# Kernel tuning notes

Measured on AMD Instinct MI355X. Metric: run time of the kernel, lower is better.

Reference implementation:

```python
import jax, jax.numpy as jnp
import numpy as np

E = 8       # num experts
TOPK = 2    # top-k routing
R = 16      # lora rank
D = 2048    # d_model
F = 5632    # ffn hidden
B, S = 4, 2048


def setup_inputs() -> dict:
    key = jax.random.key(0)
    ks = jax.random.split(key, 11)
    sc = 0.02
    return {
        "x": jax.random.normal(ks[0], (B, S, D), jnp.float32),
        "gate_w": jax.random.normal(ks[1], (E, D), jnp.float32) * sc,
        "W1": jax.random.normal(ks[2], (F, D), jnp.float32) * sc,
        "W3": jax.random.normal(ks[3], (F, D), jnp.float32) * sc,
        "W2": jax.random.normal(ks[4], (D, F), jnp.float32) * sc,
        "A1": jax.random.normal(ks[5], (E, R, D), jnp.float32) * sc,
        "B1": jax.random.normal(ks[6], (E, F, R), jnp.float32) * sc,
        "A3": jax.random.normal(ks[7], (E, R, D), jnp.float32) * sc,
        "B3": jax.random.normal(ks[8], (E, F, R), jnp.float32) * sc,
        "A2": jax.random.normal(ks[9], (E, R, F), jnp.float32) * sc,
        "B2": jax.random.normal(ks[10], (E, D, R), jnp.float32) * sc,
    }


def reference(x, gate_w, W1, W3, W2, A1, B1, A3, B3, A2, B2):
    b, s, d = x.shape
    h = x.reshape(-1, d)                              # [T, D] tokens
    # --- BasicMoe routing (fp32 softmax, top-k, renormalize) ---
    router_logits = h @ gate_w.T                      # [T, E]
    probs = jax.nn.softmax(router_logits.astype(jnp.float32), axis=-1)
    w, sel = jax.lax.top_k(probs, TOPK)               # [T, K]
    w = w / jnp.sum(w, axis=-1, keepdims=True)
    w = w.astype(h.dtype)
    # per-token per-expert combine coefficient [T, E] (0 if not routed)
    coef = jnp.sum(jax.nn.one_hot(sel, E, dtype=w.dtype) * w[..., None], axis=1)
    # --- shared base projections (expert-independent) ---
    base1 = h @ W1.T                                  # [T, F]
    base3 = h @ W3.T                                  # [T, F]
    out = jnp.zeros_like(h)
    # small fixed loop over experts; dense-masked equivalent of gather/scatter
    for e in range(E):
        u1 = base1 + (h @ A1[e].T) @ B1[e].T          # w1 + loraB1(loraA1(x))
        u3 = base3 + (h @ A3[e].T) @ B3[e].T
        g = jax.nn.silu(u1) * u3                      # SwiGLU gate
        y = g @ W2.T + (g @ A2[e].T) @ B2[e].T        # w2 + lora2
        out = out + coef[:, e:e + 1] * y
    return out.reshape(b, s, d), router_logits
```

## Files before the change

kernel.cpp:

```cpp
#include <hip/hip_runtime.h>
#include <hip/hip_bf16.h>
#include <stdint.h>

#define TT   8192
#define DD   2048
#define FF   5632
#define EE   8
#define RR   16
#define NALL 11520
#define KE   5760
#define NPAIR 16384

typedef float  f32x4  __attribute__((ext_vector_type(4)));
typedef __bf16 bf16x8 __attribute__((ext_vector_type(8)));
typedef __bf16 bf16x4 __attribute__((ext_vector_type(4)));

#define AS1CAST(p) ((__attribute__((address_space(1))) void*)(p))
#define AS3CAST(p) ((__attribute__((address_space(3))) void*)(p))

__global__ __launch_bounds__(256) void cvt_f32_bf16(const float* __restrict__ src,
                                                    __bf16* __restrict__ dst, int n4) {
    int stride = gridDim.x * 256;
    for (int i = blockIdx.x * 256 + threadIdx.x; i < n4; i += stride) {
        float4 v = ((const float4*)src)[i];
        bf16x4 o = {(__bf16)v.x, (__bf16)v.y, (__bf16)v.z, (__bf16)v.w};
        ((bf16x4*)dst)[i] = o;
    }
}

__global__ __launch_bounds__(256) void cvt_A13(const float* __restrict__ A1,
                                               const float* __restrict__ A3,
                                               __bf16* __restrict__ dst) {
    int i = blockIdx.x * 256 + threadIdx.x;
    int col4 = i & 511;
    int j = i >> 9;
    int e = j >> 5, l = j & 31;
    const float* src = (l < 16) ? (A1 + (size_t)(e * 16 + l) * DD)
                                : (A3 + (size_t)(e * 16 + (l - 16)) * DD);
    float4 v = ((const float4*)src)[col4];
    bf16x4 o = {(__bf16)v.x, (__bf16)v.y, (__bf16)v.z, (__bf16)v.w};
    ((bf16x4*)(dst + (size_t)j * DD))[col4] = o;
}

__global__ __launch_bounds__(256) void cvt_A2t(const float* __restrict__ A2,
                                               __bf16* __restrict__ A2t) {
    int i = blockIdx.x * 256 + threadIdx.x;
    int f = i % FF;
    int r = (i / FF) % RR;
    int e = i / (FF * RR);
    A2t[((size_t)e * FF + f) * RR + r] = (__bf16)A2[i];
}

__global__ __launch_bounds__(256) void cvt_W2ext(const float* __restrict__ W2,
                                                 const float* __restrict__ B2,
                                                 __bf16* __restrict__ dst) {
    const int n4 = DD * KE / 4;
    int stride = gridDim.x * 256;
    for (int i = blockIdx.x * 256 + threadIdx.x; i < n4; i += stride) {
        int j = (i % (KE / 4)) * 4;
        int d = i / (KE / 4);
        float4 v;
        if (j < FF) {
            v = *(const float4*)(W2 + (size_t)d * FF + j);
        } else {
            int o = j - FF;
            int e = o >> 4, r = o & 15;
            const float* b = B2 + ((size_t)e * DD + d) * RR + r;
            v.x = b[0]; v.y = b[1]; v.z = b[2]; v.w = b[3];
        }
        bf16x4 o4 = {(__bf16)v.x, (__bf16)v.y, (__bf16)v.z, (__bf16)v.w};
        ((bf16x4*)dst)[i] = o4;
    }
}

__global__ __launch_bounds__(256) void router_k(const float* __restrict__ x,
                                                const float* __restrict__ gw,
                                                float* __restrict__ logits,
                                                int* __restrict__ pair_e,
                                                float* __restrict__ pair_w) {
    int t = blockIdx.x * 4 + (threadIdx.x >> 6);
    int lane = threadIdx.x & 63;
    const float* xr = x + (size_t)t * DD;
    float acc[EE];
#pragma unroll
    for (int e = 0; e < EE; e++) acc[e] = 0.f;
    for (int d = lane; d < DD; d += 64) {
        float xv = xr[d];
#pragma unroll
        for (int e = 0; e < EE; e++) acc[e] += xv * gw[e * DD + d];
    }
#pragma unroll
    for (int off = 32; off > 0; off >>= 1) {
#pragma unroll
        for (int e = 0; e < EE; e++) acc[e] += __shfl_down(acc[e], off, 64);
    }
    if (lane == 0) {
        float mx = acc[0];
#pragma unroll
        for (int e = 1; e < EE; e++) mx = fmaxf(mx, acc[e]);
        float p[EE];
#pragma unroll
        for (int e = 0; e < EE; e++) p[e] = __expf(acc[e] - mx);
        int e0 = 0;
#pragma unroll
        for (int e = 1; e < EE; e++) if (p[e] > p[e0]) e0 = e;
        int e1 = (e0 == 0) ? 1 : 0;
#pragma unroll
        for (int e = 0; e < EE; e++) if (e != e0 && p[e] > p[e1]) e1 = e;
        float s = p[e0] + p[e1];
        pair_e[2 * t] = e0;     pair_e[2 * t + 1] = e1;
        pair_w[2 * t] = p[e0] / s; pair_w[2 * t + 1] = p[e1] / s;
#pragma unroll
        for (int e = 0; e < EE; e++) logits[(size_t)t * EE + e] = acc[e];
    }
}

template <int OUT_BF16>
__global__ __launch_bounds__(512, 2) void gemm256(const __bf16* __restrict__ A,
                                                  const __bf16* __restrict__ B,
                                                  void* __restrict__ Cv,
                                                  int M, int N, int K) {
    __shared__ __align__(16) __bf16 lds[8][8192];
    char* const sbase = (char*)&lds[0][0];
    const int tid = threadIdx.x;
    const int w = tid >> 6, lane = tid & 63;
    const int lrow = lane & 15, lq = lane >> 4;
    const int wr = w >> 2, wc = w & 3;

    const int gx = gridDim.x;
    const int nwg = gx * gridDim.y;
    const int orig = blockIdx.x + blockIdx.y * gx;
    const int q8 = nwg >> 3, r8 = nwg & 7;
    const int xcd = orig & 7, sid = orig >> 3;
    const int nid = (xcd < r8 ? xcd * (q8 + 1) : r8 * (q8 + 1) + (xcd - r8) * q8) + sid;
    const int m0 = (nid % gx) * 256;
    const int n0 = (nid / gx) * 256;

    const size_t ldb = (size_t)K * 2;
    const int rq0 = w * 16 + (lane >> 3);
    const int cbs = ((lane & 7) * 16) ^ (((rq0 >> 2) & 1) << 5);
    const char* gA0 = (const char*)A + (size_t)(m0 + rq0) * ldb + cbs;
    const char* gA1 = gA0 + (size_t)128 * ldb;
    const char* gB0 = (const char*)B + (size_t)(n0 + rq0) * ldb + cbs;
    const char* gB1 = gB0 + (size_t)128 * ldb;
    const int wseg = w * 2048;

    const int sb = ((lrow >> 2) & 1) << 5;
    const int aoff = lrow * 128 + ((lq * 16) ^ sb);
    const int boff = ((wc & 1) * 64 + lrow) * 128 + ((lq * 16) ^ sb);
    const int abuf = wr;
    const int bbuf = 2 + (wc >> 1);

    f32x4 acc[8][4] = {};
    bf16x8 aR[4][2], aS[4][2], bR[2][2], bS[2][2];

#define GLDS(gp, lo) __builtin_amdgcn_global_load_lds(AS1CAST((void*)(gp)), AS3CAST(sbase + (lo)), 16, 0, 0)
#define STAGEM(gp, bufmh) do { const char* _g = (gp); \
        GLDS(_g, (bufmh) * 16384 + wseg); \
        GLDS(_g + 8 * ldb, (bufmh) * 16384 + wseg + 1024); } while (0)
#define LDAf(c, i, ks) (*(const bf16x8*)(sbase + ((c) * 4 + abuf) * 16384 + aoff + (i) * 2048 + (ks) * 64))
#define LDBf(c, j, ks) (*(const bf16x8*)(sbase + ((c) * 4 + bbuf) * 16384 + boff + (j) * 2048 + (ks) * 64))
#define MM(i, j, fa, fb) acc[i][j] = __builtin_amdgcn_mfma_f32_16x16x32_bf16(fa, fb, acc[i][j], 0, 0, 0)
#define PH_MID() do { __builtin_amdgcn_s_barrier(); \
        asm volatile("s_waitcnt lgkmcnt(0)" ::: "memory"); \
        __builtin_amdgcn_sched_barrier(0); \
        __builtin_amdgcn_s_setprio(1); } while (0)
#define PH_END() do { __builtin_amdgcn_s_setprio(0); \
        __builtin_amdgcn_s_barrier(); } while (0)

#define DO4(c, kBC, kAC) do { \
    _Pragma("unroll") for (int i = 0; i < 4; i++) { aR[i][0] = LDAf(c, i, 0); aR[i][1] = LDAf(c, i, 1); } \
    _Pragma("unroll") for (int j = 0; j < 2; j++) { bR[j][0] = LDBf(c, j, 0); bR[j][1] = LDBf(c, j, 1); } \
    STAGEM(gB0 + (size_t)(kBC) * 128, ((c) ^ 1) * 4 + 2); \
    PH_MID(); \
    _Pragma("unroll") for (int i = 0; i < 4; i++) \
    _Pragma("unroll") for (int j = 0; j < 2; j++) { MM(i, j, aR[i][0], bR[j][0]); MM(i, j, aR[i][1], bR[j][1]); } \
    PH_END(); \
    _Pragma("unroll") for (int i = 0; i < 4; i++) { aS[i][0] = LDAf(c, 4 + i, 0); aS[i][1] = LDAf(c, 4 + i, 1); } \
    STAGEM(gB1 + (size_t)(kBC) * 128, ((c) ^ 1) * 4 + 3); \
    PH_MID(); \
    _Pragma("unroll") for (int i = 0; i < 4; i++) \
    _Pragma("unroll") for (int j = 0; j < 2; j++) { MM(4 + i, j, aS[i][0], bR[j][0]); MM(4 + i, j, aS[i][1], bR[j][1]); } \
    PH_END(); \
    _Pragma("unroll") for (int j = 0; j < 2; j++) { bS[j][0] = LDBf(c, 2 + j, 0); bS[j][1] = LDBf(c, 2 + j, 1); } \
    STAGEM(gA0 + (size_t)(kAC) * 128, (c) * 4 + 0); \
    PH_MID(); \
    _Pragma("unroll") for (int i = 0; i < 4; i++) \
    _Pragma("unroll") for (int j = 0; j < 2; j++) { MM(i, 2 + j, aR[i][0], bS[j][0]); MM(i, 2 + j, aR[i][1], bS[j][1]); } \
    PH_END(); \
    STAGEM(gA1 + (size_t)(kAC) * 128, (c) * 4 + 1); \
    asm volatile("s_waitcnt vmcnt(4)" ::: "memory"); \
    PH_MID(); \
    _Pragma("unroll") for (int i = 0; i < 4; i++) \
    _Pragma("unroll") for (int j = 0; j < 2; j++) { MM(4 + i, 2 + j, aS[i][0], bS[j][0]); MM(4 + i, 2 + j, aS[i][1], bS[j][1]); } \
    PH_END(); \
} while (0)

    const int NT = K >> 6;
    const int NI = NT >> 1;

    STAGEM(gA0, 0); STAGEM(gA1, 1); STAGEM(gB0, 2); STAGEM(gB1, 3);
    STAGEM(gA0 + 128, 4); STAGEM(gA1 + 128, 5);
    asm volatile("s_waitcnt vmcnt(4)" ::: "memory");
    __builtin_amdgcn_s_barrier();

    for (int it = 0; it < NI; it++) {
        int k2 = 2 * it + 2; if (k2 > NT - 1) k2 = NT - 1;
        int k3 = 2 * it + 3; if (k3 > NT - 1) k3 = NT - 1;
        DO4(0, 2 * it + 1, k2);
        DO4(1, k2, k3);
    }

    asm volatile("s_waitcnt vmcnt(0)" ::: "memory");

#undef DO4
#undef PH_END
#undef PH_MID
#undef MM
#undef LDBf
#undef LDAf
#undef STAGEM
#undef GLDS

#pragma unroll
    for (int i = 0; i < 8; i++)
#pragma unroll
        for (int j = 0; j < 4; j++)
#pragma unroll
            for (int r = 0; r < 4; r++) {
                int row = m0 + wr * 128 + i * 16 + lq * 4 + r;
                int col = n0 + wc * 64 + j * 16 + lrow;
                float v = acc[i][j][r];
                if (OUT_BF16) ((__bf16*)Cv)[(size_t)row * N + col] = (__bf16)v;
                else          ((float*)Cv)[(size_t)row * N + col] = v;
            }
}

__global__ __launch_bounds__(256) void g_build_tok(const __bf16* __restrict__ base,
                                                   const __bf16* __restrict__ B1t,
                                                   const __bf16* __restrict__ B3t,
                                                   const __bf16* __restrict__ A2t,
                                                   const int* __restrict__ pair_e,
                                                   const float* __restrict__ pair_w,
                                                   __bf16* __restrict__ G,
                                                   int t0) {
    const int wave = threadIdx.x >> 6, lane = threadIdx.x & 63;
    const int lt = blockIdx.x * 4 + wave;
    const int t = t0 + lt;
    const int e0 = pair_e[2 * t], e1 = pair_e[2 * t + 1];
    const float w0 = pair_w[2 * t], w1 = pair_w[2 * t + 1];
    const __bf16* brow = base + (size_t)lt * NALL;

    float ha1a[16], ha3a[16], ha1b[16], ha3b[16];
    {
        const bf16x8* pa = (const bf16x8*)(brow + 2 * FF + e0 * 32);
        const bf16x8* pb = (const bf16x8*)(brow + 2 * FF + e1 * 32);
        bf16x8 a0 = pa[0], a1 = pa[1], a2v = pa[2], a3v = pa[3];
        bf16x8 b0 = pb[0], b1v = pb[1], b2v = pb[2], b3v = pb[3];
#pragma unroll
        for (int r = 0; r < 8; r++) {
            ha1a[r] = (float)a0[r];  ha1a[8 + r] = (float)a1[r];
            ha3a[r] = (float)a2v[r]; ha3a[8 + r] = (float)a3v[r];
            ha1b[r] = (float)b0[r];  ha1b[8 + r] = (float)b1v[r];
            ha3b[r] = (float)b2v[r]; ha3b[8 + r] = (float)b3v[r];
        }
    }
    const __bf16* B1a = B1t + (size_t)e0 * FF * RR;
    const __bf16* B3a = B3t + (size_t)e0 * FF * RR;
    const __bf16* A2a = A2t + (size_t)e0 * FF * RR;
    const __bf16* B1b = B1t + (size_t)e1 * FF * RR;
    const __bf16* B3b = B3t + (size_t)e1 * FF * RR;
    const __bf16* A2b = A2t + (size_t)e1 * FF * RR;
    __bf16* Grow = G + (size_t)lt * KE;

    float ga0[16], ga1[16];
#pragma unroll
    for (int r = 0; r < 16; r++) { ga0[r] = 0.f; ga1[r] = 0.f; }

    for (int f = lane; f < FF; f += 64) {
        const size_t fo = (size_t)f * RR;
        const bf16x8* p;
        p = (const bf16x8*)(B1a + fo); bf16x8 b1l = p[0], b1h = p[1];
        p = (const bf16x8*)(B3a + fo); bf16x8 b3l = p[0], b3h = p[1];
        p = (const bf16x8*)(B1b + fo); bf16x8 c1l = p[0], c1h = p[1];
        p = (const bf16x8*)(B3b + fo); bf16x8 c3l = p[0], c3h = p[1];
        float bb1 = (float)brow[f], bb3 = (float)brow[FF + f];
        float u1a = bb1, u3a = bb3, u1b = bb1, u3b = bb3;
#pragma unroll
        for (int r = 0; r < 8; r++) {
            u1a += ha1a[r] * (float)b1l[r] + ha1a[8 + r] * (float)b1h[r];
            u3a += ha3a[r] * (float)b3l[r] + ha3a[8 + r] * (float)b3h[r];
            u1b += ha1b[r] * (float)c1l[r] + ha1b[8 + r] * (float)c1h[r];
            u3b += ha3b[r] * (float)c3l[r] + ha3b[8 + r] * (float)c3h[r];
        }
        float g0 = (u1a / (1.f + __expf(-u1a))) * u3a;
        float g1 = (u1b / (1.f + __expf(-u1b))) * u3b;
        Grow[f] = (__bf16)(w0 * g0 + w1 * g1);
        p = (const bf16x8*)(A2a + fo); bf16x8 a2l = p[0], a2h = p[1];
        p = (const bf16x8*)(A2b + fo); bf16x8 a4l = p[0], a4h = p[1];
#pragma unroll
        for (int r = 0; r < 8; r++) {
            ga0[r]     += g0 * (float)a2l[r];
            ga0[8 + r] += g0 * (float)a2h[r];
            ga1[r]     += g1 * (float)a4l[r];
            ga1[8 + r] += g1 * (float)a4h[r];
        }
    }
#pragma unroll
    for (int off = 32; off > 0; off >>= 1) {
#pragma unroll
        for (int r = 0; r < 16; r++) {
            ga0[r] += __shfl_down(ga0[r], off, 64);
            ga1[r] += __shfl_down(ga1[r], off, 64);
        }
    }
    if (lane == 0) {
        __bf16* tail = Grow + FF;
        bf16x8 z = {};
#pragma unroll
        for (int e = 0; e < EE; e++) {
            if (e == e0) {
                bf16x8 lo, hi;
#pragma unroll
                for (int r = 0; r < 8; r++) { lo[r] = (__bf16)(w0 * ga0[r]); hi[r] = (__bf16)(w0 * ga0[8 + r]); }
                ((bf16x8*)(tail + e * 16))[0] = lo; ((bf16x8*)(tail + e * 16))[1] = hi;
            } else if (e == e1) {
                bf16x8 lo, hi;
#pragma unroll
                for (int r = 0; r < 8; r++) { lo[r] = (__bf16)(w1 * ga1[r]); hi[r] = (__bf16)(w1 * ga1[8 + r]); }
                ((bf16x8*)(tail + e * 16))[0] = lo; ((bf16x8*)(tail + e * 16))[1] = hi;
            } else {
                ((bf16x8*)(tail + e * 16))[0] = z; ((bf16x8*)(tail + e * 16))[1] = z;
            }
        }
    }
}

extern "C" void kernel_launch(void* const* d_in, const int* in_sizes, int n_in,
                              void* d_out, int out_size, void* d_ws, size_t ws_size,
                              hipStream_t stream) {
    const float* x  = (const float*)d_in[0];
    const float* gw = (const float*)d_in[1];
    const float* W1 = (const float*)d_in[2];
    const float* W3 = (const float*)d_in[3];
    const float* W2 = (const float*)d_in[4];
    const float* A1 = (const float*)d_in[5];
    const float* B1 = (const float*)d_in[6];
    const float* A3 = (const float*)d_in[7];
    const float* B3 = (const float*)d_in[8];
    const float* A2 = (const float*)d_in[9];
    const float* B2 = (const float*)d_in[10];

    float* out    = (float*)d_out;
    float* logits = out + (size_t)TT * DD;

    char* ws = (char*)d_ws;
    size_t off = 0;
    auto carve = [&](size_t bytes) {
        char* p = ws + off;
        off += (bytes + 255) & ~(size_t)255;
        return p;
    };
    auto pad = [](size_t b) { return (b + 255) & ~(size_t)255; };

    __bf16* B1b   = (__bf16*)carve((size_t)EE * FF * RR * 2);
    __bf16* B3b   = (__bf16*)carve((size_t)EE * FF * RR * 2);
    __bf16* A2t   = (__bf16*)carve((size_t)EE * FF * RR * 2);
    int*    pair_e = (int*)carve((size_t)NPAIR * 4);
    float*  pair_w = (float*)carve((size_t)NPAIR * 4);
    char*   WREG  = carve((size_t)NALL * DD * 2);
    __bf16* W_all = (__bf16*)WREG;
    size_t base0 = off;

    int C = 0, full = 0;
    {
        const int cand[5] = {4096, 2048, 1024, 512, 256};
        for (int ci = 0; ci < 5; ci++) {
            int c = cand[ci];
            size_t need = base0 + pad((size_t)TT * KE * 2)
                        + pad((size_t)c * DD * 2) + pad((size_t)c * NALL * 2);
            if (need <= ws_size) { full = 1; C = c; break; }
        }
    }
    __bf16* Gbuf = nullptr; __bf16* base_c; __bf16* h_c; __bf16* W2e; __bf16* G_c = nullptr;
    if (full) {
        Gbuf   = (__bf16*)carve((size_t)TT * KE * 2);
        h_c    = (__bf16*)carve((size_t)C * DD * 2);
        base_c = (__bf16*)carve((size_t)C * NALL * 2);
        W2e    = (__bf16*)WREG;
    } else {
        W2e = (__bf16*)carve((size_t)DD * KE * 2);
        C = 2048;
        while (C > 256) {
            size_t need = off + pad((size_t)C * DD * 2)
                        + pad((size_t)C * NALL * 2) + pad((size_t)C * KE * 2);
            if (need <= ws_size) break;
            C >>= 1;
        }
        h_c    = (__bf16*)carve((size_t)C * DD * 2);
        base_c = (__bf16*)carve((size_t)C * NALL * 2);
        G_c    = (__bf16*)carve((size_t)C * KE * 2);
    }

    cvt_f32_bf16<<<1024, 256, 0, stream>>>(W1, W_all, FF * DD / 4);
    cvt_f32_bf16<<<1024, 256, 0, stream>>>(W3, W_all + (size_t)FF * DD, FF * DD / 4);
    cvt_A13<<<512, 256, 0, stream>>>(A1, A3, W_all + (size_t)2 * FF * DD);
    cvt_f32_bf16<<<512, 256, 0, stream>>>(B1, B1b, EE * FF * RR / 4);
    cvt_f32_bf16<<<512, 256, 0, stream>>>(B3, B3b, EE * FF * RR / 4);
    cvt_A2t<<<EE * RR * FF / 256, 256, 0, stream>>>(A2, A2t);
    if (!full) cvt_W2ext<<<2048, 256, 0, stream>>>(W2, B2, W2e);

    router_k<<<TT / 4, 256, 0, stream>>>(x, gw, logits, pair_e, pair_w);

    for (int t0 = 0; t0 < TT; t0 += C) {
        cvt_f32_bf16<<<1024, 256, 0, stream>>>(x + (size_t)t0 * DD, h_c, C * DD / 4);
        gemm256<1><<<dim3(C / 256, NALL / 256), 512, 0, stream>>>(
            h_c, W_all, base_c, C, NALL, DD);
        __bf16* Gp = full ? (Gbuf + (size_t)t0 * KE) : G_c;
        g_build_tok<<<C / 4, 256, 0, stream>>>(base_c, B1b, B3b, A2t, pair_e, pair_w, Gp, t0);
        if (!full) {
            gemm256<0><<<dim3(C / 256, DD / 256), 512, 0, stream>>>(
                G_c, W2e, out + (size_t)t0 * DD, C, DD, KE);
        }
    }

    if (full) {
        cvt_W2ext<<<2048, 256, 0, stream>>>(W2, B2, W2e);
        gemm256<0><<<dim3(TT / 256, DD / 256), 512, 0, stream>>>(
            Gbuf, W2e, out, TT, DD, KE);
    }
}
```

Measured before the change: 1.243 ms.

## Interleave per-expert LoRA tables and use bf16 dot2 in gate build

Fuses the six weight-conversion launches into one grid-stride kernel and packs B1, B3 and transposed A2 rows for each (expert, f) into one contiguous 96-byte record, so g_build_tok reads one interleaved row per expert instead of three separate arrays. The inner LoRA-B dot products now use the bf16 fdot2 builtin when available, and the f loop is unrolled by two. This aims to cut launch overhead, improve load locality, and shrink ALU work in the gate-building kernel. The cost is more complex indexing in the conversion kernel and a strided gather from A2 during packing.

```diff
diff --git a/kernel.cpp b/kernel.cpp
--- a/kernel.cpp
+++ b/kernel.cpp
@@ -14,9 +14,19 @@
 typedef float  f32x4  __attribute__((ext_vector_type(4)));
 typedef __bf16 bf16x8 __attribute__((ext_vector_type(8)));
 typedef __bf16 bf16x4 __attribute__((ext_vector_type(4)));
+typedef __bf16 bf16x2 __attribute__((ext_vector_type(2)));
 
 #define AS1CAST(p) ((__attribute__((address_space(1))) void*)(p))
 #define AS3CAST(p) ((__attribute__((address_space(3))) void*)(p))
+
+#if defined(__has_builtin)
+# if __has_builtin(__builtin_amdgcn_fdot2_f32_bf16)
+#  define HAVE_DOT2 1
+# endif
+#endif
+#ifndef HAVE_DOT2
+# define HAVE_DOT2 0
+#endif
 
 __global__ __launch_bounds__(256) void cvt_f32_bf16(const float* __restrict__ src,
                                                     __bf16* __restrict__ dst, int n4) {
@@ -28,27 +38,57 @@
     }
 }
 
-__global__ __launch_bounds__(256) void cvt_A13(const float* __restrict__ A1,
+__global__ __launch_bounds__(256) void cvt_all(const float* __restrict__ W1,
+                                               const float* __restrict__ W3,
+                                               const float* __restrict__ A1,
                                                const float* __restrict__ A3,
-                                               __bf16* __restrict__ dst) {
-    int i = blockIdx.x * 256 + threadIdx.x;
-    int col4 = i & 511;
-    int j = i >> 9;
-    int e = j >> 5, l = j & 31;
-    const float* src = (l < 16) ? (A1 + (size_t)(e * 16 + l) * DD)
-                                : (A3 + (size_t)(e * 16 + (l - 16)) * DD);
-    float4 v = ((const float4*)src)[col4];
-    bf16x4 o = {(__bf16)v.x, (__bf16)v.y, (__bf16)v.z, (__bf16)v.w};
-    ((bf16x4*)(dst + (size_t)j * DD))[col4] = o;
-}
-
-__global__ __launch_bounds__(256) void cvt_A2t(const float* __restrict__ A2,
-                                               __bf16* __restrict__ A2t) {
-    int i = blockIdx.x * 256 + threadIdx.x;
-    int f = i % FF;
-    int r = (i / FF) % RR;
-    int e = i / (FF * RR);
-    A2t[((size_t)e * FF + f) * RR + r] = (__bf16)A2[i];
+                                               const float* __restrict__ B1,
+                                               const float* __restrict__ B3,
+                                               const float* __restrict__ A2,
+                                               __bf16* __restrict__ W_all,
+                                               __bf16* __restrict__ Tbl) {
+    const int Q1 = FF * DD / 4;
+    const int QA = 256 * (DD / 4);
+    const int QT = EE * FF * 6;
+    const int NTOT = 2 * Q1 + QA + QT;
+    int stride = gridDim.x * 256;
+    for (int i = blockIdx.x * 256 + threadIdx.x; i < NTOT; i += stride) {
+        if (i < 2 * Q1) {
+            const float* s = (i < Q1) ? (W1 + (size_t)i * 4) : (W3 + (size_t)(i - Q1) * 4);
+            float4 v = *(const float4*)s;
+            bf16x4 o = {(__bf16)v.x, (__bf16)v.y, (__bf16)v.z, (__bf16)v.w};
+            ((bf16x4*)W_all)[i] = o;
+        } else if (i < 2 * Q1 + QA) {
+            int q = i - 2 * Q1;
+            int col4 = q & 511;
+            int j = q >> 9;
+            int e = j >> 5, l = j & 31;
+            const float* src = (l < 16) ? (A1 + (size_t)(e * 16 + l) * DD)
+                                        : (A3 + (size_t)(e * 16 + (l - 16)) * DD);
+            float4 v = ((const float4*)src)[col4];
+            bf16x4 o = {(__bf16)v.x, (__bf16)v.y, (__bf16)v.z, (__bf16)v.w};
+            ((bf16x4*)(W_all + (size_t)2 * FF * DD))[q] = o;
+        } else {
+            int q = i - 2 * Q1 - QA;
+            int c = q % 6;
+            int fe = q / 6;
+            int f = fe % FF, e = fe / FF;
+            __bf16* d = Tbl + (size_t)fe * 48 + c * 8;
+            bf16x8 o;
+            if (c < 4) {
+                const float* s = ((c < 2) ? B1 : B3) + ((size_t)e * FF + f) * RR + (c & 1) * 8;
+                float4 a = ((const float4*)s)[0], b = ((const float4*)s)[1];
+                o[0] = (__bf16)a.x; o[1] = (__bf16)a.y; o[2] = (__bf16)a.z; o[3] = (__bf16)a.w;
+                o[4] = (__bf16)b.x; o[5] = (__bf16)b.y; o[6] = (__bf16)b.z; o[7] = (__bf16)b.w;
+            } else {
+                int r0 = (c - 4) * 8;
+                const float* s = A2 + ((size_t)e * RR + r0) * FF + f;
+#pragma unroll
+                for (int j = 0; j < 8; j++) o[j] = (__bf16)s[(size_t)j * FF];
+            }
+            *(bf16x8*)d = o;
+        }
+    }
 }
 
 __global__ __launch_bounds__(256) void cvt_W2ext(const float* __restrict__ W2,
@@ -236,10 +276,21 @@
             }
 }
 
+__device__ __forceinline__ float dot8(bf16x8 a, bf16x8 b, float c) {
+#if HAVE_DOT2
+    const bf16x2* ap = (const bf16x2*)&a;
+    const bf16x2* bp = (const bf16x2*)&b;
+#pragma unroll
+    for (int j = 0; j < 4; j++) c = __builtin_amdgcn_fdot2_f32_bf16(ap[j], bp[j], c, false);
+#else
+#pragma unroll
+    for (int j = 0; j < 8; j++) c += (float)a[j] * (float)b[j];
+#endif
+    return c;
+}
+
 __global__ __launch_bounds__(256) void g_build_tok(const __bf16* __restrict__ base,
-                                                   const __bf16* __restrict__ B1t,
-                                                   const __bf16* __restrict__ B3t,
-                                                   const __bf16* __restrict__ A2t,
+                                                   const __bf16* __restrict__ Tbl,
                                                    const int* __restrict__ pair_e,
                                                    const float* __restrict__ pair_w,
                                                    __bf16* __restrict__ G,
@@ -251,59 +302,52 @@
     const float w0 = pair_w[2 * t], w1 = pair_w[2 * t + 1];
     const __bf16* brow = base + (size_t)lt * NALL;
 
-    float ha1a[16], ha3a[16], ha1b[16], ha3b[16];
-    {
-        const bf16x8* pa = (const bf16x8*)(brow + 2 * FF + e0 * 32);
-        const bf16x8* pb = (const bf16x8*)(brow + 2 * FF + e1 * 32);
-        bf16x8 a0 = pa[0], a1 = pa[1], a2v = pa[2], a3v = pa[3];
-        bf16x8 b0 = pb[0], b1v = pb[1], b2v = pb[2], b3v = pb[3];
-#pragma unroll
-        for (int r = 0; r < 8; r++) {
-            ha1a[r] = (float)a0[r];  ha1a[8 + r] = (float)a1[r];
-            ha3a[r] = (float)a2v[r]; ha3a[8 + r] = (float)a3v[r];
-            ha1b[r] = (float)b0[r];  ha1b[8 + r] = (float)b1v[r];
-            ha3b[r] = (float)b2v[r]; ha3b[8 + r] = (float)b3v[r];
-        }
-    }
-    const __bf16* B1a = B1t + (size_t)e0 * FF * RR;
-    const __bf16* B3a = B3t + (size_t)e0 * FF * RR;
-    const __bf16* A2a = A2t + (size_t)e0 * FF * RR;
-    const __bf16* B1b = B1t + (size_t)e1 * FF * RR;
-    const __bf16* B3b = B3t + (size_t)e1 * FF * RR;
-    const __bf16* A2b = A2t + (size_t)e1 * FF * RR;
+    const bf16x8* pa = (const bf16x8*)(brow + 2 * FF + e0 * 32);
+    const bf16x8* pb = (const bf16x8*)(brow + 2 * FF + e1 * 32);
+    bf16x8 h1a0 = pa[0], h1a1 = pa[1], h3a0 = pa[2], h3a1 = pa[3];
+    bf16x8 h1b0 = pb[0], h1b1 = pb[1], h3b0 = pb[2], h3b1 = pb[3];
+
+    const char* Ta = (const char*)Tbl + (size_t)e0 * FF * 96;
+    const char* Tb = (const char*)Tbl + (size_t)e1 * FF * 96;
     __bf16* Grow = G + (size_t)lt * KE;
 
     float ga0[16], ga1[16];
 #pragma unroll
     for (int r = 0; r < 16; r++) { ga0[r] = 0.f; ga1[r] = 0.f; }
 
+#pragma unroll 2
     for (int f = lane; f < FF; f += 64) {
-        const size_t fo = (size_t)f * RR;
-        const bf16x8* p;
-        p = (const bf16x8*)(B1a + fo); bf16x8 b1l = p[0], b1h = p[1];
-        p = (const bf16x8*)(B3a + fo); bf16x8 b3l = p[0], b3h = p[1];
-        p = (const bf16x8*)(B1b + fo); bf16x8 c1l = p[0], c1h = p[1];
-        p = (const bf16x8*)(B3b + fo); bf16x8 c3l = p[0], c3h = p[1];
-        float bb1 = (float)brow[f], bb3 = (float)brow[FF + f];
-        float u1a = bb1, u3a = bb3, u1b = bb1, u3b = bb3;
-#pragma unroll
-        for (int r = 0; r < 8; r++) {
-            u1a += ha1a[r] * (float)b1l[r] + ha1a[8 + r] * (float)b1h[r];
-            u3a += ha3a[r] * (float)b3l[r] + ha3a[8 + r] * (float)b3h[r];
-            u1b += ha1b[r] * (float)c1l[r] + ha1b[8 + r] * (float)c1h[r];
-            u3b += ha3b[r] * (float)c3l[r] + ha3b[8 + r] * (float)c3h[r];
-        }
+        const char* ra = Ta + (size_t)f * 96;
+        const char* rb = Tb + (size_t)f * 96;
+        bf16x8 b1a0 = *(const bf16x8*)(ra);
+        bf16x8 b1a1 = *(const bf16x8*)(ra + 16);
+        bf16x8 b3a0 = *(const bf16x8*)(ra + 32);
+        bf16x8 b3a1 = *(const bf16x8*)(ra + 48);
+        bf16x8 a2a0 = *(const bf16x8*)(ra + 64);
+        bf16x8 a2a1 = *(const bf16x8*)(ra + 80);
+        bf16x8 b1b0 = *(const bf16x8*)(rb);
+        bf16x8 b1b1 = *(const bf16x8*)(rb + 16);
+        bf16x8 b3b0 = *(const bf16x8*)(rb + 32);
+        bf16x8 b3b1 = *(const bf16x8*)(rb + 48);
+        bf16x8 a2b0 = *(const bf16x8*)(rb + 64);
+        bf16x8 a2b1 = *(const bf16x8*)(rb + 80);
+
+        float bb1 = (float)brow[f];
+        float bb3 = (float)brow[FF + f];
+        float u1a = dot8(h1a1, b1a1, dot8(h1a0, b1a0, bb1));
+        float u3a = dot8(h3a1, b3a1, dot8(h3a0, b3a0, bb3));
+        float u1b = dot8(h1b1, b1b1, dot8(h1b0, b1b0, bb1));
+        float u3b = dot8(h3b1, b3b1, dot8(h3b0, b3b0, bb3));
+
         float g0 = (u1a / (1.f + __expf(-u1a))) * u3a;
         float g1 = (u1b / (1.f + __expf(-u1b))) * u3b;
         Grow[f] = (__bf16)(w0 * g0 + w1 * g1);
-        p = (const bf16x8*)(A2a + fo); bf16x8 a2l = p[0], a2h = p[1];
-        p = (const bf16x8*)(A2b + fo); bf16x8 a4l = p[0], a4h = p[1];
 #pragma unroll
         for (int r = 0; r < 8; r++) {
-            ga0[r]     += g0 * (float)a2l[r];
-            ga0[8 + r] += g0 * (float)a2h[r];
-            ga1[r]     += g1 * (float)a4l[r];
-            ga1[8 + r] += g1 * (float)a4h[r];
+            ga0[r]     += g0 * (float)a2a0[r];
+            ga0[8 + r] += g0 * (float)a2a1[r];
+            ga1[r]     += g1 * (float)a2b0[r];
+            ga1[8 + r] += g1 * (float)a2b1[r];
         }
     }
 #pragma unroll
@@ -363,9 +407,7 @@
     };
     auto pad = [](size_t b) { return (b + 255) & ~(size_t)255; };
 
-    __bf16* B1b   = (__bf16*)carve((size_t)EE * FF * RR * 2);
-    __bf16* B3b   = (__bf16*)carve((size_t)EE * FF * RR * 2);
-    __bf16* A2t   = (__bf16*)carve((size_t)EE * FF * RR * 2);
+    __bf16* Tbl   = (__bf16*)carve((size_t)EE * FF * 48 * 2);
     int*    pair_e = (int*)carve((size_t)NPAIR * 4);
     float*  pair_w = (float*)carve((size_t)NPAIR * 4);
     char*   WREG  = carve((size_t)NALL * DD * 2);
@@ -402,12 +444,7 @@
         G_c    = (__bf16*)carve((size_t)C * KE * 2);
     }
 
-    cvt_f32_bf16<<<1024, 256, 0, stream>>>(W1, W_all, FF * DD / 4);
-    cvt_f32_bf16<<<1024, 256, 0, stream>>>(W3, W_all + (size_t)FF * DD, FF * DD / 4);
-    cvt_A13<<<512, 256, 0, stream>>>(A1, A3, W_all + (size_t)2 * FF * DD);
-    cvt_f32_bf16<<<512, 256, 0, stream>>>(B1, B1b, EE * FF * RR / 4);
-    cvt_f32_bf16<<<512, 256, 0, stream>>>(B3, B3b, EE * FF * RR / 4);
-    cvt_A2t<<<EE * RR * FF / 256, 256, 0, stream>>>(A2, A2t);
+    cvt_all<<<4096, 256, 0, stream>>>(W1, W3, A1, A3, B1, B3, A2, W_all, Tbl);
     if (!full) cvt_W2ext<<<2048, 256, 0, stream>>>(W2, B2, W2e);
 
     router_k<<<TT / 4, 256, 0, stream>>>(x, gw, logits, pair_e, pair_w);
@@ -417,7 +454,7 @@
         gemm256<1><<<dim3(C / 256, NALL / 256), 512, 0, stream>>>(
             h_c, W_all, base_c, C, NALL, DD);
         __bf16* Gp = full ? (Gbuf + (size_t)t0 * KE) : G_c;
-        g_build_tok<<<C / 4, 256, 0, stream>>>(base_c, B1b, B3b, A2t, pair_e, pair_w, Gp, t0);
+        g_build_tok<<<C / 4, 256, 0, stream>>>(base_c, Tbl, pair_e, pair_w, Gp, t0);
         if (!full) {
             gemm256<0><<<dim3(C / 256, DD / 256), 512, 0, stream>>>(
                 G_c, W2e, out + (size_t)t0 * DD, C, DD, KE);
```

Result: no change. 1.227 ms (-1.3%).
